# Performance work log

Hardware: AMD Instinct MI355X
Metric: run time of the kernel (lower is better)

Reference implementation:

```python
import jax, jax.numpy as jnp
import numpy as np
from jax import lax

STRENGTH = 1.0
NORMALIZE = True


def setup_inputs() -> dict:
    key = jax.random.key(0)
    k1, k2 = jax.random.split(key)
    hidden_states = jax.random.normal(k1, (8, 4096, 1024), dtype=jnp.float32)
    # probe_weight is [k, hidden]; Q = orth(probe_weight.T) -> [hidden, k] orthonormal columns
    pw = jax.random.normal(k2, (1024, 16), dtype=jnp.float32)
    Q, _ = jnp.linalg.qr(pw)  # [hidden, k], orthonormal columns
    return {"hidden_states": hidden_states, "Q": Q}


def reference(hidden_states, Q):
    if NORMALIZE:
        old_norms = jnp.linalg.norm(hidden_states, axis=2, keepdims=True)  # [B,S,1]
    # Sequential Gram-Schmidt removal per direction (column of Q), as in the torch loop.
    def step(h, q):  # h: [B,S,H], q: [H]
        coef = jnp.einsum('bsh,h->bs', h, q)          # projection coefficient
        h = h - STRENGTH * coef[..., None] * q        # subtract component along q
        return h, None
    h, _ = lax.scan(step, hidden_states, Q.T)          # scan over k directions
    if NORMALIZE:
        norms = jnp.linalg.norm(h, axis=2, keepdims=True)
        h = h / norms * old_norms
    return h
```

## Files before the change

### kernel.cpp

```cpp
#include <hip/hip_runtime.h>
#include <hip/hip_bf16.h>

constexpr int HID = 1024;
constexpr int KD  = 16;
constexpr int TM  = 16;
constexpr int NW  = 4;

typedef short bf16x8 __attribute__((ext_vector_type(8)));
typedef float f32x4  __attribute__((ext_vector_type(4)));

__device__ __forceinline__ short f2b(float x) {
    __hip_bfloat16 b = __float2bfloat16(x);
    return *reinterpret_cast<short*>(&b);
}
__device__ __forceinline__ float b2f(short s) {
    return __uint_as_float(((unsigned int)(unsigned short)s) << 16);
}

__global__ void q_setup(const float* __restrict__ Qf,
                        short* __restrict__ Qt, short* __restrict__ Qa) {
    const int idx = blockIdx.x*256 + threadIdx.x;
    if (idx < 16*HID) {
        const int r = idx >> 10, k = idx & 1023;
        Qt[idx] = f2b(Qf[k*KD + r]);

        const int gs = idx >> 4, dir = idx & 15;
        const int jslot = gs >> 4, rr = gs & 15;
        const int w = jslot >> 4, jl = jslot & 15;
        const int p = jl >> 1, odd = jl & 1;
        const int col = w*256 + p*32 + (rr >> 2)*8 + odd*4 + (rr & 3);
        Qa[idx] = f2b(Qf[col*KD + dir]);
    }
}

__global__ __launch_bounds__(NW*64)
void probe_removal_fused(const float* __restrict__ H,
                         const short* __restrict__ Qt,
                         const short* __restrict__ Qa,
                         float* __restrict__ out)
{
    const int lane = threadIdx.x & 63;
    const int w    = threadIdx.x >> 6;
    const int r    = lane & 15;
    const int q    = lane >> 4;
    const int tile = blockIdx.x;

    __shared__ __align__(16) float ctr[NW][TM][20];
    __shared__ float s2p[NW][TM];

    const float* hrow   = H + (size_t)tile*TM*HID + r*HID;
    const int   colbase = w*256 + q*8;

    bf16x8 bq[8];
    #pragma unroll
    for (int kt = 0; kt < 8; ++kt)
        bq[kt] = *reinterpret_cast<const bf16x8*>(Qt + r*1024 + colbase + kt*32);

    bf16x8 af[8];
    f32x4 acc0 = {0.f,0.f,0.f,0.f}, acc1 = {0.f,0.f,0.f,0.f};
    float s2 = 0.f;
    #pragma unroll
    for (int kt = 0; kt < 8; ++kt) {
        const float4 x = *reinterpret_cast<const float4*>(hrow + colbase + kt*32);
        const float4 y = *reinterpret_cast<const float4*>(hrow + colbase + kt*32 + 4);
        s2 = fmaf(x.x,x.x, fmaf(x.y,x.y, fmaf(x.z,x.z, fmaf(x.w,x.w, s2))));
        s2 = fmaf(y.x,y.x, fmaf(y.y,y.y, fmaf(y.z,y.z, fmaf(y.w,y.w, s2))));
        bf16x8 a;
        a[0]=f2b(x.x); a[1]=f2b(x.y); a[2]=f2b(x.z); a[3]=f2b(x.w);
        a[4]=f2b(y.x); a[5]=f2b(y.y); a[6]=f2b(y.z); a[7]=f2b(y.w);
        af[kt] = a;
        if (kt & 1) acc1 = __builtin_amdgcn_mfma_f32_16x16x32_bf16(a, bq[kt], acc1, 0, 0, 0);
        else        acc0 = __builtin_amdgcn_mfma_f32_16x16x32_bf16(a, bq[kt], acc0, 0, 0, 0);
    }
    const f32x4 acc = acc0 + acc1;
    s2 += __shfl_xor(s2, 16);
    s2 += __shfl_xor(s2, 32);

    #pragma unroll
    for (int i = 0; i < 4; ++i) ctr[w][q*4 + i][r] = acc[i];
    if (q == 0) s2p[w][r] = s2;

    __syncthreads();

    float cf[8] = {0,0,0,0,0,0,0,0};
    if (q < 2) {
        #pragma unroll
        for (int w2 = 0; w2 < NW; ++w2) {
            const float4 a = *reinterpret_cast<const float4*>(&ctr[w2][r][q*8]);
            const float4 b = *reinterpret_cast<const float4*>(&ctr[w2][r][q*8 + 4]);
            cf[0]+=a.x; cf[1]+=a.y; cf[2]+=a.z; cf[3]+=a.w;
            cf[4]+=b.x; cf[5]+=b.y; cf[6]+=b.z; cf[7]+=b.w;
        }
    }
    float s2tot = 0.f;
    #pragma unroll
    for (int w2 = 0; w2 < NW; ++w2) s2tot += s2p[w2][r];

    float sc2 = 0.f;
    #pragma unroll
    for (int i = 0; i < 8; ++i) sc2 = fmaf(cf[i], cf[i], sc2);
    sc2 += __shfl_xor(sc2, 16);
    sc2 += __shfl_xor(sc2, 32);
    const float scale = rsqrtf(fmaxf(1.0f - sc2 / s2tot, 1e-20f));

    bf16x8 pb;
    #pragma unroll
    for (int i = 0; i < 8; ++i) pb[i] = f2b(cf[i]);

    float* orow = out + (size_t)tile*TM*HID + r*HID + w*256;
    const f32x4 zero4 = {0.f,0.f,0.f,0.f};
    #pragma unroll
    for (int p = 0; p < 8; ++p) {
        bf16x8 a0, a1;
        if (q < 2) {
            a0 = *reinterpret_cast<const bf16x8*>(Qa + ((w*16 + 2*p    )*16 + r)*KD + q*8);
            a1 = *reinterpret_cast<const bf16x8*>(Qa + ((w*16 + 2*p + 1)*16 + r)*KD + q*8);
        } else {
            #pragma unroll
            for (int i = 0; i < 8; ++i) { a0[i] = 0; a1[i] = 0; }
        }
        const f32x4 d0 = __builtin_amdgcn_mfma_f32_16x16x32_bf16(a0, pb, zero4, 0, 0, 0);
        const f32x4 d1 = __builtin_amdgcn_mfma_f32_16x16x32_bf16(a1, pb, zero4, 0, 0, 0);
        f32x4 o0, o1;
        #pragma unroll
        for (int ii = 0; ii < 4; ++ii) {
            o0[ii] = (b2f(af[p][ii])     - d0[ii]) * scale;
            o1[ii] = (b2f(af[p][4 + ii]) - d1[ii]) * scale;
        }
        *reinterpret_cast<f32x4*>(orow + p*32 + q*8)     = o0;
        *reinterpret_cast<f32x4*>(orow + p*32 + q*8 + 4) = o1;
    }
}

extern "C" void kernel_launch(void* const* d_in, const int* in_sizes, int n_in,
                              void* d_out, int out_size, void* d_ws, size_t ws_size,
                              hipStream_t stream) {
    const float* H  = (const float*)d_in[0];
    const float* Qf = (const float*)d_in[1];
    float* outp     = (float*)d_out;
    const int nrows  = in_sizes[0] / HID;
    const int ntiles = nrows / TM;

    short* Qt = (short*)d_ws;
    short* Qa = Qt + 16*HID;

    hipLaunchKernelGGL(q_setup, dim3(64), dim3(256), 0, stream, Qf, Qt, Qa);
    hipLaunchKernelGGL(probe_removal_fused, dim3(ntiles), dim3(NW*64), 0, stream,
                       H, Qt, Qa, outp);
}
```

Baseline: 61.76 us.

## Double-buffer hidden-state tiles into LDS with async global_load_lds over persistent blocks

```diff
diff --git a/kernel.cpp b/kernel.cpp
--- a/kernel.cpp
+++ b/kernel.cpp
@@ -5,6 +5,7 @@
 constexpr int KD  = 16;
 constexpr int TM  = 16;
 constexpr int NW  = 4;
+constexpr int TPB = 8;
 
 typedef short bf16x8 __attribute__((ext_vector_type(8)));
 typedef float f32x4  __attribute__((ext_vector_type(4)));
@@ -23,7 +24,6 @@
     if (idx < 16*HID) {
         const int r = idx >> 10, k = idx & 1023;
         Qt[idx] = f2b(Qf[k*KD + r]);
-
         const int gs = idx >> 4, dir = idx & 15;
         const int jslot = gs >> 4, rr = gs & 15;
         const int w = jslot >> 4, jl = jslot & 15;
@@ -33,102 +33,154 @@
     }
 }
 
+#define SCHED_FENCE() __builtin_amdgcn_sched_barrier(0)
+
+__device__ __forceinline__ void stage_tile(float* ldsBuf, const float* Hbase,
+                                           int w, int lane) {
+    #pragma unroll
+    for (int i = 0; i < 16; ++i) {
+        const int rr = w*4 + (i >> 2);
+        const int qq = i & 3;
+        const int s  = qq*64 + lane;
+        const float* g = Hbase + rr*1024 + ((s ^ (rr & 7)) << 2);
+        const float* l = ldsBuf + rr*1024 + qq*256;
+        __builtin_amdgcn_global_load_lds(
+            (const __attribute__((address_space(1))) void*)g,
+            (__attribute__((address_space(3))) void*)l, 16, 0, 0);
+    }
+}
+
 __global__ __launch_bounds__(NW*64)
-void probe_removal_fused(const float* __restrict__ H,
-                         const short* __restrict__ Qt,
-                         const short* __restrict__ Qa,
-                         float* __restrict__ out)
+void probe_removal_dma(const float* __restrict__ H,
+                       const short* __restrict__ Qt,
+                       const short* __restrict__ Qa,
+                       float* __restrict__ out)
 {
     const int lane = threadIdx.x & 63;
     const int w    = threadIdx.x >> 6;
     const int r    = lane & 15;
     const int q    = lane >> 4;
-    const int tile = blockIdx.x;
-
+
+    __shared__ __align__(16) float Hb[2][TM][HID];
     __shared__ __align__(16) float ctr[NW][TM][20];
     __shared__ float s2p[NW][TM];
 
-    const float* hrow   = H + (size_t)tile*TM*HID + r*HID;
-    const int   colbase = w*256 + q*8;
+    const int tile0 = blockIdx.x * TPB;
 
     bf16x8 bq[8];
     #pragma unroll
     for (int kt = 0; kt < 8; ++kt)
-        bq[kt] = *reinterpret_cast<const bf16x8*>(Qt + r*1024 + colbase + kt*32);
-
-    bf16x8 af[8];
-    f32x4 acc0 = {0.f,0.f,0.f,0.f}, acc1 = {0.f,0.f,0.f,0.f};
-    float s2 = 0.f;
-    #pragma unroll
-    for (int kt = 0; kt < 8; ++kt) {
-        const float4 x = *reinterpret_cast<const float4*>(hrow + colbase + kt*32);
-        const float4 y = *reinterpret_cast<const float4*>(hrow + colbase + kt*32 + 4);
-        s2 = fmaf(x.x,x.x, fmaf(x.y,x.y, fmaf(x.z,x.z, fmaf(x.w,x.w, s2))));
-        s2 = fmaf(y.x,y.x, fmaf(y.y,y.y, fmaf(y.z,y.z, fmaf(y.w,y.w, s2))));
-        bf16x8 a;
-        a[0]=f2b(x.x); a[1]=f2b(x.y); a[2]=f2b(x.z); a[3]=f2b(x.w);
-        a[4]=f2b(y.x); a[5]=f2b(y.y); a[6]=f2b(y.z); a[7]=f2b(y.w);
-        af[kt] = a;
-        if (kt & 1) acc1 = __builtin_amdgcn_mfma_f32_16x16x32_bf16(a, bq[kt], acc1, 0, 0, 0);
-        else        acc0 = __builtin_amdgcn_mfma_f32_16x16x32_bf16(a, bq[kt], acc0, 0, 0, 0);
-    }
-    const f32x4 acc = acc0 + acc1;
-    s2 += __shfl_xor(s2, 16);
-    s2 += __shfl_xor(s2, 32);
-
-    #pragma unroll
-    for (int i = 0; i < 4; ++i) ctr[w][q*4 + i][r] = acc[i];
-    if (q == 0) s2p[w][r] = s2;
-
-    __syncthreads();
-
-    float cf[8] = {0,0,0,0,0,0,0,0};
-    if (q < 2) {
-        #pragma unroll
-        for (int w2 = 0; w2 < NW; ++w2) {
-            const float4 a = *reinterpret_cast<const float4*>(&ctr[w2][r][q*8]);
-            const float4 b = *reinterpret_cast<const float4*>(&ctr[w2][r][q*8 + 4]);
-            cf[0]+=a.x; cf[1]+=a.y; cf[2]+=a.z; cf[3]+=a.w;
-            cf[4]+=b.x; cf[5]+=b.y; cf[6]+=b.z; cf[7]+=b.w;
-        }
-    }
-    float s2tot = 0.f;
-    #pragma unroll
-    for (int w2 = 0; w2 < NW; ++w2) s2tot += s2p[w2][r];
-
-    float sc2 = 0.f;
-    #pragma unroll
-    for (int i = 0; i < 8; ++i) sc2 = fmaf(cf[i], cf[i], sc2);
-    sc2 += __shfl_xor(sc2, 16);
-    sc2 += __shfl_xor(sc2, 32);
-    const float scale = rsqrtf(fmaxf(1.0f - sc2 / s2tot, 1e-20f));
-
-    bf16x8 pb;
-    #pragma unroll
-    for (int i = 0; i < 8; ++i) pb[i] = f2b(cf[i]);
-
-    float* orow = out + (size_t)tile*TM*HID + r*HID + w*256;
-    const f32x4 zero4 = {0.f,0.f,0.f,0.f};
+        bq[kt] = *reinterpret_cast<const bf16x8*>(Qt + r*1024 + w*256 + q*8 + kt*32);
+    bf16x8 aq0[8], aq1[8];
     #pragma unroll
     for (int p = 0; p < 8; ++p) {
-        bf16x8 a0, a1;
         if (q < 2) {
-            a0 = *reinterpret_cast<const bf16x8*>(Qa + ((w*16 + 2*p    )*16 + r)*KD + q*8);
-            a1 = *reinterpret_cast<const bf16x8*>(Qa + ((w*16 + 2*p + 1)*16 + r)*KD + q*8);
+            aq0[p] = *reinterpret_cast<const bf16x8*>(Qa + ((w*16 + 2*p    )*16 + r)*KD + q*8);
+            aq1[p] = *reinterpret_cast<const bf16x8*>(Qa + ((w*16 + 2*p + 1)*16 + r)*KD + q*8);
         } else {
             #pragma unroll
-            for (int i = 0; i < 8; ++i) { a0[i] = 0; a1[i] = 0; }
-        }
-        const f32x4 d0 = __builtin_amdgcn_mfma_f32_16x16x32_bf16(a0, pb, zero4, 0, 0, 0);
-        const f32x4 d1 = __builtin_amdgcn_mfma_f32_16x16x32_bf16(a1, pb, zero4, 0, 0, 0);
-        f32x4 o0, o1;
-        #pragma unroll
-        for (int ii = 0; ii < 4; ++ii) {
-            o0[ii] = (b2f(af[p][ii])     - d0[ii]) * scale;
-            o1[ii] = (b2f(af[p][4 + ii]) - d1[ii]) * scale;
-        }
-        *reinterpret_cast<f32x4*>(orow + p*32 + q*8)     = o0;
-        *reinterpret_cast<f32x4*>(orow + p*32 + q*8 + 4) = o1;
+            for (int i = 0; i < 8; ++i) { aq0[p][i] = 0; aq1[p][i] = 0; }
+        }
+    }
+    SCHED_FENCE();
+
+    stage_tile(&Hb[0][0][0], H + (size_t)tile0*TM*HID, w, lane);
+    SCHED_FENCE();
+    stage_tile(&Hb[1][0][0], H + (size_t)(tile0+1)*TM*HID, w, lane);
+    SCHED_FENCE();
+    asm volatile("s_waitcnt vmcnt(16)" ::: "memory");
+    SCHED_FENCE();
+    __builtin_amdgcn_s_barrier();
+
+    #pragma unroll
+    for (int t = 0; t < TPB; ++t) {
+        const int cur = t & 1;
+        const char* HbC = (const char*)&Hb[cur][0][0];
+
+        bf16x8 af[8];
+        f32x4 acc0 = {0.f,0.f,0.f,0.f}, acc1 = {0.f,0.f,0.f,0.f};
+        float s2 = 0.f;
+        #pragma unroll
+        for (int kt = 0; kt < 8; ++kt) {
+            const int P  = w*64 + kt*8 + q*2;
+            const int sx = P ^ (r & 7);
+            const float4 x = *(const float4*)(HbC + r*4096 + sx*16);
+            const float4 y = *(const float4*)(HbC + r*4096 + (sx^1)*16);
+            s2 = fmaf(x.x,x.x, fmaf(x.y,x.y, fmaf(x.z,x.z, fmaf(x.w,x.w, s2))));
+            s2 = fmaf(y.x,y.x, fmaf(y.y,y.y, fmaf(y.z,y.z, fmaf(y.w,y.w, s2))));
+            bf16x8 a;
+            a[0]=f2b(x.x); a[1]=f2b(x.y); a[2]=f2b(x.z); a[3]=f2b(x.w);
+            a[4]=f2b(y.x); a[5]=f2b(y.y); a[6]=f2b(y.z); a[7]=f2b(y.w);
+            af[kt] = a;
+            if (kt & 1) acc1 = __builtin_amdgcn_mfma_f32_16x16x32_bf16(a, bq[kt], acc1, 0, 0, 0);
+            else        acc0 = __builtin_amdgcn_mfma_f32_16x16x32_bf16(a, bq[kt], acc0, 0, 0, 0);
+        }
+        const f32x4 acc = acc0 + acc1;
+        s2 += __shfl_xor(s2, 16);
+        s2 += __shfl_xor(s2, 32);
+
+        #pragma unroll
+        for (int i = 0; i < 4; ++i) ctr[w][q*4 + i][r] = acc[i];
+        if (q == 0) s2p[w][r] = s2;
+
+        asm volatile("s_waitcnt lgkmcnt(0)" ::: "memory");
+        SCHED_FENCE();
+        __builtin_amdgcn_s_barrier();
+        SCHED_FENCE();
+
+        if (t + 2 < TPB)
+            stage_tile(&Hb[cur][0][0], H + (size_t)(tile0+t+2)*TM*HID, w, lane);
+        SCHED_FENCE();
+
+        float cf[8] = {0,0,0,0,0,0,0,0};
+        if (q < 2) {
+            #pragma unroll
+            for (int w2 = 0; w2 < NW; ++w2) {
+                const float4 a = *reinterpret_cast<const float4*>(&ctr[w2][r][q*8]);
+                const float4 b = *reinterpret_cast<const float4*>(&ctr[w2][r][q*8 + 4]);
+                cf[0]+=a.x; cf[1]+=a.y; cf[2]+=a.z; cf[3]+=a.w;
+                cf[4]+=b.x; cf[5]+=b.y; cf[6]+=b.z; cf[7]+=b.w;
+            }
+        }
+        float s2tot = 0.f;
+        #pragma unroll
+        for (int w2 = 0; w2 < NW; ++w2) s2tot += s2p[w2][r];
+
+        float sc2 = 0.f;
+        #pragma unroll
+        for (int i = 0; i < 8; ++i) sc2 = fmaf(cf[i], cf[i], sc2);
+        sc2 += __shfl_xor(sc2, 16);
+        sc2 += __shfl_xor(sc2, 32);
+        const float scale = rsqrtf(fmaxf(1.0f - sc2 / s2tot, 1e-20f));
+
+        bf16x8 pb;
+        #pragma unroll
+        for (int i = 0; i < 8; ++i) pb[i] = f2b(cf[i]);
+
+        float* orow = out + (size_t)(tile0+t)*TM*HID + r*HID + w*256;
+        const f32x4 zero4 = {0.f,0.f,0.f,0.f};
+        #pragma unroll
+        for (int p = 0; p < 8; ++p) {
+            const f32x4 d0 = __builtin_amdgcn_mfma_f32_16x16x32_bf16(aq0[p], pb, zero4, 0, 0, 0);
+            const f32x4 d1 = __builtin_amdgcn_mfma_f32_16x16x32_bf16(aq1[p], pb, zero4, 0, 0, 0);
+            f32x4 o0, o1;
+            #pragma unroll
+            for (int ii = 0; ii < 4; ++ii) {
+                o0[ii] = (b2f(af[p][ii])     - d0[ii]) * scale;
+                o1[ii] = (b2f(af[p][4 + ii]) - d1[ii]) * scale;
+            }
+            *reinterpret_cast<f32x4*>(orow + p*32 + q*8)     = o0;
+            *reinterpret_cast<f32x4*>(orow + p*32 + q*8 + 4) = o1;
+        }
+        SCHED_FENCE();
+
+        if (t < TPB-2)       { asm volatile("s_waitcnt vmcnt(32)" ::: "memory"); }
+        else if (t == TPB-2) { asm volatile("s_waitcnt vmcnt(16)" ::: "memory"); }
+        if (t < TPB-1) {
+            SCHED_FENCE();
+            __builtin_amdgcn_s_barrier();
+            SCHED_FENCE();
+        }
     }
 }
 
@@ -145,6 +197,7 @@
     short* Qa = Qt + 16*HID;
 
     hipLaunchKernelGGL(q_setup, dim3(64), dim3(256), 0, stream, Qf, Qt, Qa);
-    hipLaunchKernelGGL(probe_removal_fused, dim3(ntiles), dim3(NW*64), 0, stream,
+
+    hipLaunchKernelGGL(probe_removal_dma, dim3(ntiles / TPB), dim3(NW*64), 0, stream,
                        H, Qt, Qa, outp);
 }
```

After: 58.12 us. 1.06x faster.
